# Kernel tuning notes

Measured on AMD Instinct MI355X. Metric: run time of the kernel, lower is better.

The kernel has to match this reference:

```python
import jax, jax.numpy as jnp
import numpy as np
import math

IN_FEATURES = 4096
OUT_FEATURES = 4096
NUM_COMPONENTS = 256
TWO_PI = 2.0 * math.pi


def setup_inputs() -> dict:
    key = jax.random.key(0)
    k1, k2, k3, k4 = jax.random.split(key, 4)
    x = jax.random.normal(k1, (4096, IN_FEATURES), dtype=jnp.float32)
    mus = jax.random.uniform(k2, (NUM_COMPONENTS, 2), dtype=jnp.float32)
    log_vars = -3.0 - jax.random.uniform(k3, (NUM_COMPONENTS, 2), dtype=jnp.float32)
    weights = jax.random.uniform(k4, (NUM_COMPONENTS,), dtype=jnp.float32) / NUM_COMPONENTS
    return {"x": x, "mus": mus, "log_vars": log_vars, "weights": weights}


def reference(x, mus, log_vars, weights):
    in_features = x.shape[1]
    x_in_idx = jnp.linspace(0.0, 1.0, in_features, dtype=jnp.float32)    # [I]
    x_out_idx = jnp.linspace(0.0, 1.0, OUT_FEATURES, dtype=jnp.float32)  # [O]
    vars_ = jnp.exp(log_vars)  # [M, 2]

    # Input-side Gaussian basis, fused with 1/sqrt(2*pi*var) and component weight: [I, M]
    d_in = (x_in_idx[:, None] - mus[None, :, 0]) ** 2
    G_in = jnp.exp(-d_in / (2.0 * vars_[None, :, 0])) / jnp.sqrt(TWO_PI * vars_[None, :, 0]) * weights[None, :]
    C = x @ G_in  # [B, M]

    # Output-side Gaussian pdf (Normal(mu1, sigma1).log_prob(x_out).exp()): [M, O]
    d_out = (x_out_idx[None, :] - mus[:, 1:2]) ** 2
    G_out = jnp.exp(-d_out / (2.0 * vars_[:, 1:2])) / jnp.sqrt(TWO_PI * vars_[:, 1:2])

    x_out = (C @ G_out) / (in_features * jnp.sum(weights))  # [B, O]
    return x_out
```

## Files before the change

### kernel.cpp

```cpp
#include <hip/hip_runtime.h>
#include <hip/hip_bf16.h>
#include <math.h>

#define IN_FEAT 4096
#define OUT_FEAT 4096
#define NCOMP 256
#define BATCH 4096
#define TWO_PI_F 6.28318530717958647692f

typedef __attribute__((ext_vector_type(8))) short short8;
typedef __attribute__((ext_vector_type(8))) __bf16 bf16x8;
typedef __attribute__((ext_vector_type(4))) float f32x4;

__device__ __forceinline__ ushort f2b(float f) {
  union { float f; unsigned u; } v; v.f = f;
  unsigned r = (v.u + 0x7fffu + ((v.u >> 16) & 1u)) >> 16;
  return (ushort)r;
}

__device__ __forceinline__ float b2f(short s) {
  union { unsigned u; float f; } v; v.u = ((unsigned)(ushort)s) << 16;
  return v.f;
}

__device__ __forceinline__ bf16x8 ld_frag(const void* p) {
  short8 s = *(const short8*)p;
  return __builtin_bit_cast(bf16x8, s);
}

__device__ __forceinline__ bf16x8 cvt8(float4 a, float4 b) {
  short8 h;
  h[0] = (short)f2b(a.x); h[1] = (short)f2b(a.y);
  h[2] = (short)f2b(a.z); h[3] = (short)f2b(a.w);
  h[4] = (short)f2b(b.x); h[5] = (short)f2b(b.y);
  h[6] = (short)f2b(b.z); h[7] = (short)f2b(b.w);
  return __builtin_bit_cast(bf16x8, h);
}

__device__ __forceinline__ void gload_lds16(const ushort* g, ushort* l) {
  __builtin_amdgcn_global_load_lds(
      (const __attribute__((address_space(1))) void*)g,
      (__attribute__((address_space(3))) void*)l, 16, 0, 0);
}

__global__ void wsum_kernel(const float* __restrict__ w, float* __restrict__ wsum) {
  float v = w[threadIdx.x];
  #pragma unroll
  for (int off = 32; off > 0; off >>= 1) v += __shfl_down(v, off);
  __shared__ float s[4];
  if ((threadIdx.x & 63) == 0) s[threadIdx.x >> 6] = v;
  __syncthreads();
  if (threadIdx.x == 0) wsum[0] = s[0] + s[1] + s[2] + s[3];
}

__global__ __launch_bounds__(256) void prep_kernel(
    const float* __restrict__ mus, const float* __restrict__ lvs,
    const float* __restrict__ w, const float* __restrict__ wsum,
    ushort* __restrict__ Gt, ushort* __restrict__ GoT) {
  int idx = blockIdx.x * 256 + threadIdx.x;
  if (idx < NCOMP * IN_FEAT) {
    int m = idx >> 12, i = idx & (IN_FEAT - 1);
    float v = expf(lvs[2 * m]);
    float d = (float)i * (1.0f / (IN_FEAT - 1)) - mus[2 * m];
    float g = expf(-d * d * (0.5f / v)) * rsqrtf(TWO_PI_F * v) * w[m];
    Gt[idx] = f2b(g);
  } else {
    idx -= NCOMP * IN_FEAT;
    int o = idx >> 8, m = idx & (NCOMP - 1);
    float v = expf(lvs[2 * m + 1]);
    float d = (float)o * (1.0f / (OUT_FEAT - 1)) - mus[2 * m + 1];
    float scale = 1.0f / ((float)IN_FEAT * wsum[0]);
    float g = expf(-d * d * (0.5f / v)) * rsqrtf(TWO_PI_F * v) * scale;
    GoT[idx] = f2b(g);
  }
}

__global__ __launch_bounds__(256, 2) void gemm1_kernel(
    const float* __restrict__ x, const ushort* __restrict__ Gt,
    ushort* __restrict__ Cpart) {
  __shared__ __align__(16) ushort Bs[32768];
  const int tid = threadIdx.x, wid = tid >> 6, lane = tid & 63;
  const int m0 = blockIdx.x * 64;
  const int kr = IN_FEAT / gridDim.y;
  const int kb0 = blockIdx.y * kr;
  const int NT = kr >> 6;

  f32x4 acc[16] = {};

  const int brow = lane >> 2;
  const int bswz = (((lane & 3) ^ ((lane >> 3) & 3)) << 3);
  const int fswz = ((lane >> 4) << 4) ^ ((((lane & 15) >> 1) & 3) << 4);

  const float* xp = &x[(size_t)(m0 + wid * 16 + (lane & 15)) * IN_FEAT +
                       kb0 + ((lane >> 4) << 3)];

  #define G1_STAGE(buf, kb)                                                  \
    _Pragma("unroll")                                                        \
    for (int q = 0; q < 8; ++q) {                                            \
      int c = wid * 8 + q, s_ = c >> 4, nb = c & 15;                         \
      gload_lds16(&Gt[(size_t)(nb * 16 + brow) * IN_FEAT + (kb) + s_ * 32 + bswz], \
                  &Bs[(buf) * 16384 + s_ * 8192 + nb * 512]);                \
    }

  G1_STAGE(0, kb0)
  __syncthreads();

  for (int t = 0; t < NT; ++t) {
    float4 u0 = *(const float4*)(xp + t * 64);
    float4 u1 = *(const float4*)(xp + t * 64 + 4);
    float4 u2 = *(const float4*)(xp + t * 64 + 32);
    float4 u3 = *(const float4*)(xp + t * 64 + 36);
    if (t + 1 < NT) { G1_STAGE((t + 1) & 1, kb0 + (t + 1) * 64) }

    const char* Bb = (const char*)&Bs[(t & 1) * 16384];
    bf16x8 af0 = cvt8(u0, u1);
    #pragma unroll
    for (int j = 0; j < 16; ++j) {
      bf16x8 bf = ld_frag(Bb + (j * 16 + (lane & 15)) * 64 + fswz);
      acc[j] = __builtin_amdgcn_mfma_f32_16x16x32_bf16(af0, bf, acc[j], 0, 0, 0);
    }
    bf16x8 af1 = cvt8(u2, u3);
    #pragma unroll
    for (int j = 0; j < 16; ++j) {
      bf16x8 bf = ld_frag(Bb + 16384 + (j * 16 + (lane & 15)) * 64 + fswz);
      acc[j] = __builtin_amdgcn_mfma_f32_16x16x32_bf16(af1, bf, acc[j], 0, 0, 0);
    }
    __syncthreads();
  }
  #undef G1_STAGE

  ushort* Cp = Cpart + (size_t)blockIdx.y * ((size_t)BATCH * NCOMP);
  #pragma unroll
  for (int j = 0; j < 16; ++j)
    #pragma unroll
    for (int r = 0; r < 4; ++r) {
      int row = m0 + wid * 16 + (lane >> 4) * 4 + r;
      int col = j * 16 + (lane & 15);
      Cp[(size_t)row * NCOMP + col] = f2b(acc[j][r]);
    }
}

__global__ __launch_bounds__(256) void reduce_kernel(
    const ushort* __restrict__ Cp, ushort* __restrict__ Cb, int nsplit) {
  size_t i = ((size_t)blockIdx.x * 256 + threadIdx.x) * 8;
  float s[8] = {0.f, 0.f, 0.f, 0.f, 0.f, 0.f, 0.f, 0.f};
  for (int p = 0; p < nsplit; ++p) {
    short8 v = *(const short8*)&Cp[(size_t)p * BATCH * NCOMP + i];
    #pragma unroll
    for (int e = 0; e < 8; ++e) s[e] += b2f(v[e]);
  }
  short8 h;
  #pragma unroll
  for (int e = 0; e < 8; ++e) h[e] = (short)f2b(s[e]);
  *(short8*)&Cb[i] = h;
}

__global__ __launch_bounds__(256) void gemm2_kernel(
    const ushort* __restrict__ Cb, const ushort* __restrict__ GoT,
    float* __restrict__ out) {
  __shared__ __align__(16) ushort As[128 * 32];
  __shared__ __align__(16) ushort Bs[128 * 32];
  const int tid = threadIdx.x, wid = tid >> 6, lane = tid & 63;
  const int m0 = blockIdx.y * 128, n0 = blockIdx.x * 128;
  const int wr = (wid >> 1) * 64, wc = (wid & 1) * 64;
  const int srow = lane >> 2;
  const int srck = (((lane & 3) ^ ((lane >> 3) & 3)) << 3);
  const int fswz = ((lane >> 4) << 4) ^ ((((lane & 15) >> 1) & 3) << 4);

  f32x4 acc[4][4] = {};

  for (int k0 = 0; k0 < NCOMP; k0 += 32) {
    #pragma unroll
    for (int q = 0; q < 2; ++q) {
      int cw = wid * 2 + q;
      int row = cw * 16 + srow;
      gload_lds16(&Cb[(size_t)(m0 + row) * NCOMP + k0 + srck], &As[cw * 512]);
      gload_lds16(&GoT[(size_t)(n0 + row) * NCOMP + k0 + srck], &Bs[cw * 512]);
    }
    __syncthreads();

    bf16x8 af[4], bf[4];
    #pragma unroll
    for (int i = 0; i < 4; ++i)
      af[i] = ld_frag((const char*)As + (wr + i * 16 + (lane & 15)) * 64 + fswz);
    #pragma unroll
    for (int j = 0; j < 4; ++j)
      bf[j] = ld_frag((const char*)Bs + (wc + j * 16 + (lane & 15)) * 64 + fswz);
    #pragma unroll
    for (int i = 0; i < 4; ++i)
      #pragma unroll
      for (int j = 0; j < 4; ++j)
        acc[i][j] = __builtin_amdgcn_mfma_f32_16x16x32_bf16(af[i], bf[j], acc[i][j], 0, 0, 0);
    __syncthreads();
  }

  #pragma unroll
  for (int i = 0; i < 4; ++i)
    #pragma unroll
    for (int r = 0; r < 4; ++r) {
      int row = m0 + wr + i * 16 + (lane >> 4) * 4 + r;
      #pragma unroll
      for (int j = 0; j < 4; ++j)
        out[(size_t)row * OUT_FEAT + n0 + wc + j * 16 + (lane & 15)] = acc[i][j][r];
    }
}

extern "C" void kernel_launch(void* const* d_in, const int* in_sizes, int n_in,
                              void* d_out, int out_size, void* d_ws, size_t ws_size,
                              hipStream_t stream) {
  const float* x   = (const float*)d_in[0];
  const float* mus = (const float*)d_in[1];
  const float* lvs = (const float*)d_in[2];
  const float* w   = (const float*)d_in[3];
  float* out = (float*)d_out;

  ushort* Gt  = (ushort*)d_ws;
  ushort* GoT = Gt  + (size_t)NCOMP * IN_FEAT;
  ushort* Cb  = GoT + (size_t)OUT_FEAT * NCOMP;
  ushort* Cpart = Cb + (size_t)BATCH * NCOMP;

  size_t base = (size_t)6 * 1024 * 1024;
  int nsplit = 8;
  while (nsplit > 1 &&
         ws_size < base + (size_t)nsplit * 2 * 1024 * 1024 + 64)
    nsplit >>= 1;
  float* wsum = (float*)(Cpart + (size_t)nsplit * BATCH * NCOMP);

  wsum_kernel<<<1, 256, 0, stream>>>(w, wsum);
  prep_kernel<<<(NCOMP * IN_FEAT + OUT_FEAT * NCOMP) / 256, 256, 0, stream>>>(
      mus, lvs, w, wsum, Gt, GoT);
  gemm1_kernel<<<dim3(BATCH / 64, nsplit), 256, 0, stream>>>(x, Gt, Cpart);
  reduce_kernel<<<(BATCH * NCOMP / 8) / 256, 256, 0, stream>>>(Cpart, Cb, nsplit);
  gemm2_kernel<<<dim3(OUT_FEAT / 128, BATCH / 128), 256, 0, stream>>>(Cb, GoT, out);
}
```

Baseline: 61.54 us.

## Restructure GEMM pipeline: smaller K tiles, more splits, fold weight-sum into GEMM2

Removes the separate weight-sum kernel and computes the normalization scale inside gemm2, applying it at the output store. gemm1 now stages x through LDS in bf16 with a 32-wide K tile and a smaller LDS footprint, raising occupancy to 4 blocks. It uses templated split counts up to 16, and the reduce writes in place into partition 0. gemm2 gains double-buffered LDS staging so the next tile loads while the current one computes. More splits add partial-sum traffic, and the reduce is skipped when there is only one split.

```diff
diff --git a/kernel.cpp b/kernel.cpp
--- a/kernel.cpp
+++ b/kernel.cpp
@@ -28,13 +28,13 @@
   return __builtin_bit_cast(bf16x8, s);
 }
 
-__device__ __forceinline__ bf16x8 cvt8(float4 a, float4 b) {
+__device__ __forceinline__ short8 cvt8(float4 a, float4 b) {
   short8 h;
   h[0] = (short)f2b(a.x); h[1] = (short)f2b(a.y);
   h[2] = (short)f2b(a.z); h[3] = (short)f2b(a.w);
   h[4] = (short)f2b(b.x); h[5] = (short)f2b(b.y);
   h[6] = (short)f2b(b.z); h[7] = (short)f2b(b.w);
-  return __builtin_bit_cast(bf16x8, h);
+  return h;
 }
 
 __device__ __forceinline__ void gload_lds16(const ushort* g, ushort* l) {
@@ -43,19 +43,9 @@
       (__attribute__((address_space(3))) void*)l, 16, 0, 0);
 }
 
-__global__ void wsum_kernel(const float* __restrict__ w, float* __restrict__ wsum) {
-  float v = w[threadIdx.x];
-  #pragma unroll
-  for (int off = 32; off > 0; off >>= 1) v += __shfl_down(v, off);
-  __shared__ float s[4];
-  if ((threadIdx.x & 63) == 0) s[threadIdx.x >> 6] = v;
-  __syncthreads();
-  if (threadIdx.x == 0) wsum[0] = s[0] + s[1] + s[2] + s[3];
-}
-
 __global__ __launch_bounds__(256) void prep_kernel(
     const float* __restrict__ mus, const float* __restrict__ lvs,
-    const float* __restrict__ w, const float* __restrict__ wsum,
+    const float* __restrict__ w,
     ushort* __restrict__ Gt, ushort* __restrict__ GoT) {
   int idx = blockIdx.x * 256 + threadIdx.x;
   if (idx < NCOMP * IN_FEAT) {
@@ -69,21 +59,21 @@
     int o = idx >> 8, m = idx & (NCOMP - 1);
     float v = expf(lvs[2 * m + 1]);
     float d = (float)o * (1.0f / (OUT_FEAT - 1)) - mus[2 * m + 1];
-    float scale = 1.0f / ((float)IN_FEAT * wsum[0]);
-    float g = expf(-d * d * (0.5f / v)) * rsqrtf(TWO_PI_F * v) * scale;
+    float g = expf(-d * d * (0.5f / v)) * rsqrtf(TWO_PI_F * v);
     GoT[idx] = f2b(g);
   }
 }
 
-__global__ __launch_bounds__(256, 2) void gemm1_kernel(
+template<int NS>
+__global__ __launch_bounds__(256, 4) void gemm1_kernel(
     const float* __restrict__ x, const ushort* __restrict__ Gt,
     ushort* __restrict__ Cpart) {
-  __shared__ __align__(16) ushort Bs[32768];
+  constexpr int KR = IN_FEAT / NS;
+  constexpr int NT = KR / 32;
+  __shared__ __align__(16) ushort lds[2 * 10240];
   const int tid = threadIdx.x, wid = tid >> 6, lane = tid & 63;
   const int m0 = blockIdx.x * 64;
-  const int kr = IN_FEAT / gridDim.y;
-  const int kb0 = blockIdx.y * kr;
-  const int NT = kr >> 6;
+  const int kb0 = blockIdx.y * KR;
 
   f32x4 acc[16] = {};
 
@@ -91,60 +81,64 @@
   const int bswz = (((lane & 3) ^ ((lane >> 3) & 3)) << 3);
   const int fswz = ((lane >> 4) << 4) ^ ((((lane & 15) >> 1) & 3) << 4);
 
-  const float* xp = &x[(size_t)(m0 + wid * 16 + (lane & 15)) * IN_FEAT +
-                       kb0 + ((lane >> 4) << 3)];
-
-  #define G1_STAGE(buf, kb)                                                  \
+  const int arow = tid >> 2, aslot = tid & 3;
+  const float* asrc = &x[(size_t)(m0 + arow) * IN_FEAT + kb0 + aslot * 8];
+  const int abyte = arow * 64 + ((aslot << 4) ^ (((arow >> 1) & 3) << 4));
+
+  #define STAGE_B(buf, kb)                                                   \
     _Pragma("unroll")                                                        \
-    for (int q = 0; q < 8; ++q) {                                            \
-      int c = wid * 8 + q, s_ = c >> 4, nb = c & 15;                         \
-      gload_lds16(&Gt[(size_t)(nb * 16 + brow) * IN_FEAT + (kb) + s_ * 32 + bswz], \
-                  &Bs[(buf) * 16384 + s_ * 8192 + nb * 512]);                \
-    }
-
-  G1_STAGE(0, kb0)
+    for (int q = 0; q < 4; ++q) {                                            \
+      int nb = wid * 4 + q;                                                  \
+      gload_lds16(&Gt[(size_t)(nb * 16 + brow) * IN_FEAT + (kb) + bswz],     \
+                  &lds[(buf) * 10240 + nb * 512]);                           \
+    }
+
+  STAGE_B(0, kb0)
+  {
+    float4 a0 = *(const float4*)asrc;
+    float4 a1 = *(const float4*)(asrc + 4);
+    *(short8*)((char*)lds + 16384 + abyte) = cvt8(a0, a1);
+  }
   __syncthreads();
 
   for (int t = 0; t < NT; ++t) {
-    float4 u0 = *(const float4*)(xp + t * 64);
-    float4 u1 = *(const float4*)(xp + t * 64 + 4);
-    float4 u2 = *(const float4*)(xp + t * 64 + 32);
-    float4 u3 = *(const float4*)(xp + t * 64 + 36);
-    if (t + 1 < NT) { G1_STAGE((t + 1) & 1, kb0 + (t + 1) * 64) }
-
-    const char* Bb = (const char*)&Bs[(t & 1) * 16384];
-    bf16x8 af0 = cvt8(u0, u1);
-    #pragma unroll
-    for (int j = 0; j < 16; ++j) {
-      bf16x8 bf = ld_frag(Bb + (j * 16 + (lane & 15)) * 64 + fswz);
-      acc[j] = __builtin_amdgcn_mfma_f32_16x16x32_bf16(af0, bf, acc[j], 0, 0, 0);
-    }
-    bf16x8 af1 = cvt8(u2, u3);
-    #pragma unroll
-    for (int j = 0; j < 16; ++j) {
-      bf16x8 bf = ld_frag(Bb + 16384 + (j * 16 + (lane & 15)) * 64 + fswz);
-      acc[j] = __builtin_amdgcn_mfma_f32_16x16x32_bf16(af1, bf, acc[j], 0, 0, 0);
-    }
+    float4 px0, px1;
+    if (t + 1 < NT) {
+      STAGE_B((t + 1) & 1, kb0 + (t + 1) * 32)
+      px0 = *(const float4*)(asrc + (t + 1) * 32);
+      px1 = *(const float4*)(asrc + (t + 1) * 32 + 4);
+    }
+    const char* base = (const char*)lds + (t & 1) * 20480;
+    bf16x8 af = ld_frag(base + 16384 + (wid * 16 + (lane & 15)) * 64 + fswz);
+    #pragma unroll
+    for (int nj = 0; nj < 16; ++nj) {
+      bf16x8 bf = ld_frag(base + (nj * 16 + (lane & 15)) * 64 + fswz);
+      acc[nj] = __builtin_amdgcn_mfma_f32_16x16x32_bf16(af, bf, acc[nj], 0, 0, 0);
+    }
+    if (t + 1 < NT)
+      *(short8*)((char*)lds + ((t + 1) & 1) * 20480 + 16384 + abyte) =
+          cvt8(px0, px1);
     __syncthreads();
   }
-  #undef G1_STAGE
+  #undef STAGE_B
 
   ushort* Cp = Cpart + (size_t)blockIdx.y * ((size_t)BATCH * NCOMP);
   #pragma unroll
-  for (int j = 0; j < 16; ++j)
+  for (int nj = 0; nj < 16; ++nj)
     #pragma unroll
     for (int r = 0; r < 4; ++r) {
       int row = m0 + wid * 16 + (lane >> 4) * 4 + r;
-      int col = j * 16 + (lane & 15);
-      Cp[(size_t)row * NCOMP + col] = f2b(acc[j][r]);
-    }
-}
-
-__global__ __launch_bounds__(256) void reduce_kernel(
-    const ushort* __restrict__ Cp, ushort* __restrict__ Cb, int nsplit) {
+      int col = nj * 16 + (lane & 15);
+      Cp[(size_t)row * NCOMP + col] = f2b(acc[nj][r]);
+    }
+}
+
+template<int NS>
+__global__ __launch_bounds__(256) void reduce_kernel(ushort* __restrict__ Cp) {
   size_t i = ((size_t)blockIdx.x * 256 + threadIdx.x) * 8;
-  float s[8] = {0.f, 0.f, 0.f, 0.f, 0.f, 0.f, 0.f, 0.f};
-  for (int p = 0; p < nsplit; ++p) {
+  float s[8] = {};
+  #pragma unroll
+  for (int p = 0; p < NS; ++p) {
     short8 v = *(const short8*)&Cp[(size_t)p * BATCH * NCOMP + i];
     #pragma unroll
     for (int e = 0; e < 8; ++e) s[e] += b2f(v[e]);
@@ -152,40 +146,53 @@
   short8 h;
   #pragma unroll
   for (int e = 0; e < 8; ++e) h[e] = (short)f2b(s[e]);
-  *(short8*)&Cb[i] = h;
-}
-
-__global__ __launch_bounds__(256) void gemm2_kernel(
+  *(short8*)&Cp[i] = h;
+}
+
+__global__ __launch_bounds__(256, 4) void gemm2_kernel(
     const ushort* __restrict__ Cb, const ushort* __restrict__ GoT,
-    float* __restrict__ out) {
-  __shared__ __align__(16) ushort As[128 * 32];
-  __shared__ __align__(16) ushort Bs[128 * 32];
+    const float* __restrict__ w, float* __restrict__ out) {
+  __shared__ __align__(16) ushort lds[2 * 8192];
   const int tid = threadIdx.x, wid = tid >> 6, lane = tid & 63;
   const int m0 = blockIdx.y * 128, n0 = blockIdx.x * 128;
   const int wr = (wid >> 1) * 64, wc = (wid & 1) * 64;
-  const int srow = lane >> 2;
-  const int srck = (((lane & 3) ^ ((lane >> 3) & 3)) << 3);
+
+  float4 wv = *(const float4*)&w[lane * 4];
+  float s = wv.x + wv.y + wv.z + wv.w;
+  #pragma unroll
+  for (int off = 32; off > 0; off >>= 1) s += __shfl_xor(s, off);
+  const float scale = 1.0f / ((float)IN_FEAT * s);
+
+  const int brow = lane >> 2;
+  const int bswz = (((lane & 3) ^ ((lane >> 3) & 3)) << 3);
   const int fswz = ((lane >> 4) << 4) ^ ((((lane & 15) >> 1) & 3) << 4);
 
   f32x4 acc[4][4] = {};
 
-  for (int k0 = 0; k0 < NCOMP; k0 += 32) {
-    #pragma unroll
-    for (int q = 0; q < 2; ++q) {
-      int cw = wid * 2 + q;
-      int row = cw * 16 + srow;
-      gload_lds16(&Cb[(size_t)(m0 + row) * NCOMP + k0 + srck], &As[cw * 512]);
-      gload_lds16(&GoT[(size_t)(n0 + row) * NCOMP + k0 + srck], &Bs[cw * 512]);
-    }
-    __syncthreads();
-
+  #define STAGE2(buf, k0)                                                    \
+    _Pragma("unroll")                                                        \
+    for (int q = 0; q < 2; ++q) {                                            \
+      int c = wid * 2 + q;                                                   \
+      int row = c * 16 + brow;                                               \
+      gload_lds16(&Cb[(size_t)(m0 + row) * NCOMP + (k0) + bswz],             \
+                  &lds[(buf) * 8192 + c * 512]);                             \
+      gload_lds16(&GoT[(size_t)(n0 + row) * NCOMP + (k0) + bswz],            \
+                  &lds[(buf) * 8192 + 4096 + c * 512]);                      \
+    }
+
+  STAGE2(0, 0)
+  __syncthreads();
+
+  for (int t = 0; t < 8; ++t) {
+    if (t < 7) STAGE2((t + 1) & 1, (t + 1) * 32)
+    const char* base = (const char*)lds + (t & 1) * 16384;
     bf16x8 af[4], bf[4];
     #pragma unroll
     for (int i = 0; i < 4; ++i)
-      af[i] = ld_frag((const char*)As + (wr + i * 16 + (lane & 15)) * 64 + fswz);
+      af[i] = ld_frag(base + (wr + i * 16 + (lane & 15)) * 64 + fswz);
     #pragma unroll
     for (int j = 0; j < 4; ++j)
-      bf[j] = ld_frag((const char*)Bs + (wc + j * 16 + (lane & 15)) * 64 + fswz);
+      bf[j] = ld_frag(base + 8192 + (wc + j * 16 + (lane & 15)) * 64 + fswz);
     #pragma unroll
     for (int i = 0; i < 4; ++i)
       #pragma unroll
@@ -193,6 +200,7 @@
         acc[i][j] = __builtin_amdgcn_mfma_f32_16x16x32_bf16(af[i], bf[j], acc[i][j], 0, 0, 0);
     __syncthreads();
   }
+  #undef STAGE2
 
   #pragma unroll
   for (int i = 0; i < 4; ++i)
@@ -201,7 +209,8 @@
       int row = m0 + wr + i * 16 + (lane >> 4) * 4 + r;
       #pragma unroll
       for (int j = 0; j < 4; ++j)
-        out[(size_t)row * OUT_FEAT + n0 + wc + j * 16 + (lane & 15)] = acc[i][j][r];
+        out[(size_t)row * OUT_FEAT + n0 + wc + j * 16 + (lane & 15)] =
+            acc[i][j][r] * scale;
     }
 }
 
@@ -216,20 +225,33 @@
 
   ushort* Gt  = (ushort*)d_ws;
   ushort* GoT = Gt  + (size_t)NCOMP * IN_FEAT;
-  ushort* Cb  = GoT + (size_t)OUT_FEAT * NCOMP;
-  ushort* Cpart = Cb + (size_t)BATCH * NCOMP;
-
-  size_t base = (size_t)6 * 1024 * 1024;
-  int nsplit = 8;
-  while (nsplit > 1 &&
-         ws_size < base + (size_t)nsplit * 2 * 1024 * 1024 + 64)
-    nsplit >>= 1;
-  float* wsum = (float*)(Cpart + (size_t)nsplit * BATCH * NCOMP);
-
-  wsum_kernel<<<1, 256, 0, stream>>>(w, wsum);
+  ushort* Cpart = GoT + (size_t)OUT_FEAT * NCOMP;
+
+  const size_t MiB = 1024 * 1024;
+  int nsplit = 16;
+  while (nsplit > 1 && ws_size < 4 * MiB + (size_t)nsplit * 2 * MiB) nsplit >>= 1;
+
   prep_kernel<<<(NCOMP * IN_FEAT + OUT_FEAT * NCOMP) / 256, 256, 0, stream>>>(
-      mus, lvs, w, wsum, Gt, GoT);
-  gemm1_kernel<<<dim3(BATCH / 64, nsplit), 256, 0, stream>>>(x, Gt, Cpart);
-  reduce_kernel<<<(BATCH * NCOMP / 8) / 256, 256, 0, stream>>>(Cpart, Cb, nsplit);
-  gemm2_kernel<<<dim3(OUT_FEAT / 128, BATCH / 128), 256, 0, stream>>>(Cb, GoT, out);
-}
+      mus, lvs, w, Gt, GoT);
+
+  dim3 g1(BATCH / 64, nsplit);
+  switch (nsplit) {
+    case 16: gemm1_kernel<16><<<g1, 256, 0, stream>>>(x, Gt, Cpart);
+             reduce_kernel<16><<<BATCH * NCOMP / 8 / 256, 256, 0, stream>>>(Cpart);
+             break;
+    case 8:  gemm1_kernel<8><<<g1, 256, 0, stream>>>(x, Gt, Cpart);
+             reduce_kernel<8><<<BATCH * NCOMP / 8 / 256, 256, 0, stream>>>(Cpart);
+             break;
+    case 4:  gemm1_kernel<4><<<g1, 256, 0, stream>>>(x, Gt, Cpart);
+             reduce_kernel<4><<<BATCH * NCOMP / 8 / 256, 256, 0, stream>>>(Cpart);
+             break;
+    case 2:  gemm1_kernel<2><<<g1, 256, 0, stream>>>(x, Gt, Cpart);
+             reduce_kernel<2><<<BATCH * NCOMP / 8 / 256, 256, 0, stream>>>(Cpart);
+             break;
+    default: gemm1_kernel<1><<<g1, 256, 0, stream>>>(x, Gt, Cpart);
+             break;
+  }
+
+  gemm2_kernel<<<dim3(OUT_FEAT / 128, BATCH / 128), 256, 0, stream>>>(
+      Cpart, GoT, w, out);
+}
```

Result: no change. 60.77 us (-1.3%).
